# Performance work log

Hardware: AMD Instinct MI355X
Metric: run time of the kernel (lower is better)

## Reference

```python
import jax, jax.numpy as jnp
import numpy as np

NUM_CLASSES = 2
KS = 5  # kernel_size
EPS = 1e-8  # torch cosine_similarity eps


def setup_inputs() -> dict:
    key = jax.random.key(0)
    k1, k2, k3 = jax.random.split(key, 3)
    b, c, h, w = 8, 256, 128, 128
    er_input = jax.random.normal(k1, (b, c, h, w), dtype=jnp.float32)
    seg_label = jax.random.randint(k2, (b, h, w), 0, 2, dtype=jnp.int32)
    gt_boundary_seg = jax.random.randint(k3, (b, h, w), 0, 2, dtype=jnp.int32)
    return {"er_input": er_input, "seg_label": seg_label, "gt_boundary_seg": gt_boundary_seg}


def _context_loss(er_input, seg_label, gt_boundary_seg):
    # seg_label / gt_boundary_seg already at er_input spatial size (nearest interp is identity)
    b, c, h, w = er_input.shape
    r = KS // 2
    seg0 = jnp.where(seg_label == 255, 0, seg_label)
    gtb0 = jnp.where(gt_boundary_seg == 255, 0, gt_boundary_seg)
    gt_b = gtb0 * seg0                                  # [b,h,w] boundary pixels on fg classes
    interior = jnp.zeros((h, w), bool).at[r:h - r, r:w - r].set(True)
    valid = (gt_b > 0) & interior                       # pixels whose 5x5 window is in-bounds
    include = (gt_b > 0).any(axis=(1, 2))               # images contributing to scale_num
    cnt = valid.sum(axis=(1, 2)).astype(er_input.dtype)  # [b]

    norm = jnp.maximum(jnp.sqrt((er_input * er_input).sum(axis=1)), EPS)  # [b,h,w]
    validf = valid.astype(er_input.dtype)
    total = jnp.zeros((b,), dtype=er_input.dtype)
    n_shift = 0
    for dy in range(-r, r + 1):
        for dx in range(-r, r + 1):
            if dy == 0 and dx == 0:
                continue
            n_shift += 1
            # value at p+ (dy,dx) brought to p; valid pixels are interior so no wrap issue
            feat_s = jnp.roll(er_input, (-dy, -dx), axis=(2, 3))
            norm_s = jnp.roll(norm, (-dy, -dx), axis=(1, 2))
            seg_s = jnp.roll(seg_label, (-dy, -dx), axis=(1, 2))
            dot = (er_input * feat_s).sum(axis=1)       # [b,h,w]
            cos = dot / (norm * norm_s)
            # one_hot(seg,256)[:num_classes] dot product == labels equal AND label < num_classes
            labsim = ((seg_label == seg_s) & (seg_label < NUM_CLASSES)).astype(er_input.dtype)
            sq = (cos - labsim) ** 2
            # mse_loss over selected boundary pixels of image i
            total = total + (sq * validf).sum(axis=(1, 2)) / jnp.maximum(cnt, 1.0)
    loss_i = total / float(n_shift)                     # per-image context_loss_pi / 24
    scale_num = jnp.maximum(include.sum(), 1)
    return (loss_i * include.astype(loss_i.dtype)).sum() / scale_num.astype(loss_i.dtype)


def reference(er_input, seg_label, gt_boundary_seg):
    return _context_loss(er_input, seg_label, gt_boundary_seg)
```

## Files before the change

### kernel.cpp

```cpp
#include <hip/hip_runtime.h>
#include <math.h>

#define BATCH 8
#define CH    256
#define H     128
#define W     128
#define PLANE (H * W)
#define NPIX  (BATCH * PLANE)
#define NSHIFT 12
#define NMAPS  13
#define NCHUNK 4
#define CPC    (CH / NCHUNK)
#define NZ4    (NMAPS * NPIX / 4)

static __device__ __constant__ int S_DY[NSHIFT] = {0,0,1,1,1,1,1,2,2,2,2,2};
static __device__ __constant__ int S_DX[NSHIFT] = {1,2,-2,-1,0,1,2,-2,-1,0,1,2};

#define NCORRB (BATCH * 32 * NCHUNK)
#define NSTATB (BATCH * 64)

__device__ __forceinline__ void fma4(float& acc, const float4& a, const float4& b) {
    acc = fmaf(a.x, b.x, acc);
    acc = fmaf(a.y, b.y, acc);
    acc = fmaf(a.z, b.z, acc);
    acc = fmaf(a.w, b.w, acc);
}

__global__ __launch_bounds__(256) void k_prep(float4* __restrict__ comb4,
                                              int* __restrict__ cnt,
                                              int* __restrict__ inc,
                                              float* __restrict__ out) {
    int i = blockIdx.x * 256 + threadIdx.x;
    if (i < NZ4) comb4[i] = make_float4(0.f, 0.f, 0.f, 0.f);
    if (blockIdx.x == 0) {
        int t = threadIdx.x;
        if (t < 8) { cnt[t] = 0; inc[t] = 0; }
        if (t == 0) out[0] = 0.0f;
    }
}

__global__ __launch_bounds__(256, 4) void k_corr(const float* __restrict__ er,
                                                 const int* __restrict__ seg,
                                                 const int* __restrict__ gtb,
                                                 float* __restrict__ comb,
                                                 int* __restrict__ cnt,
                                                 int* __restrict__ inc) {
    __shared__ float4 lds[6][132];
    int t = threadIdx.x;

    if (blockIdx.x >= NCORRB) {
        int blk2 = blockIdx.x - NCORRB;
        int b = blk2 >> 6;
        int i = (blk2 & 63) * 256 + t;
        int my_cnt = 0, my_any = 0;
        {
            int s = seg[b * PLANE + i];
            int g = gtb[b * PLANE + i];
            int s0 = (s == 255) ? 0 : s;
            int g0 = (g == 255) ? 0 : g;
            if (s0 > 0 && g0 > 0) {
                my_any = 1;
                int y = i >> 7, x = i & 127;
                if (y >= 2 && y < H - 2 && x >= 2 && x < W - 2) my_cnt = 1;
            }
        }
        for (int o = 32; o > 0; o >>= 1) {
            my_cnt += __shfl_down(my_cnt, o, 64);
            my_any |= __shfl_down(my_any, o, 64);
        }
        __shared__ int sc[4], sa[4];
        int lane = t & 63, wid = t >> 6;
        if (lane == 0) { sc[wid] = my_cnt; sa[wid] = my_any; }
        __syncthreads();
        if (t == 0) {
            int c = sc[0] + sc[1] + sc[2] + sc[3];
            int a = sa[0] | sa[1] | sa[2] | sa[3];
            if (c) atomicAdd(&cnt[b], c);
            if (a) atomicOr(&inc[b], 1);
        }
        return;
    }

    int blk = blockIdx.x;
    int chunk = blk & 3;
    int tile  = (blk >> 2) & 31;
    int b     = blk >> 7;
    int y0 = tile * 4;
    int c0 = chunk * CPC;
    int r = t >> 7;
    int x = t & 127;

    if (t < 24) {
        int row = t >> 2, col = t & 3;
        int xs = (col < 2) ? col : (col + 128);
        lds[row][xs] = make_float4(0.f, 0.f, 0.f, 0.f);
    }

    float accA[13], accB[13];
#pragma unroll
    for (int i = 0; i < 13; i++) { accA[i] = 0.0f; accB[i] = 0.0f; }

    const float* base = er + (size_t)b * CH * PLANE;

    float pf[3][4];
    auto load_quad = [&](int c) {
#pragma unroll
        for (int k = 0; k < 3; ++k) {
            int s = t + k * 256;
            int row = s >> 7;
            int xs = s & 127;
            int y = y0 + row;
            if (y < H) {
                const float* p0 = base + (size_t)c * PLANE + y * W + xs;
                pf[k][0] = p0[0];
                pf[k][1] = p0[PLANE];
                pf[k][2] = p0[2 * PLANE];
                pf[k][3] = p0[3 * PLANE];
            } else {
                pf[k][0] = 0.f; pf[k][1] = 0.f; pf[k][2] = 0.f; pf[k][3] = 0.f;
            }
        }
    };

    load_quad(c0);
    const int iters = CPC / 4;
    for (int it = 0; it < iters; ++it) {
        __syncthreads();
#pragma unroll
        for (int k = 0; k < 3; ++k) {
            int s = t + k * 256;
            int row = s >> 7;
            int xs = s & 127;
            lds[row][xs + 2] = make_float4(pf[k][0], pf[k][1], pf[k][2], pf[k][3]);
        }
        __syncthreads();
        if (it + 1 < iters) load_quad(c0 + 4 * (it + 1));

        const float4* lp = &lds[2 * r][x + 2];
        float4 cA = lp[0];
        float4 cB = lp[132];
        {
            float4 v1 = lp[1], v2 = lp[2];
            fma4(accA[0], cA, cA);
            fma4(accA[1], cA, v1);
            fma4(accA[2], cA, v2);
        }
        {
            float4 m2 = lp[130], m1 = lp[131], p1 = lp[133], p2 = lp[134];
            fma4(accA[3], cA, m2);
            fma4(accA[4], cA, m1);
            fma4(accA[5], cA, cB);
            fma4(accA[6], cA, p1);
            fma4(accA[7], cA, p2);
            fma4(accB[0], cB, cB);
            fma4(accB[1], cB, p1);
            fma4(accB[2], cB, p2);
        }
        {
            float4 m2 = lp[262], m1 = lp[263], v0 = lp[264], p1 = lp[265], p2 = lp[266];
            fma4(accA[8],  cA, m2);
            fma4(accA[9],  cA, m1);
            fma4(accA[10], cA, v0);
            fma4(accA[11], cA, p1);
            fma4(accA[12], cA, p2);
            fma4(accB[3], cB, m2);
            fma4(accB[4], cB, m1);
            fma4(accB[5], cB, v0);
            fma4(accB[6], cB, p1);
            fma4(accB[7], cB, p2);
        }
        {
            float4 m2 = lp[394], m1 = lp[395], v0 = lp[396], p1 = lp[397], p2 = lp[398];
            fma4(accB[8],  cB, m2);
            fma4(accB[9],  cB, m1);
            fma4(accB[10], cB, v0);
            fma4(accB[11], cB, p1);
            fma4(accB[12], cB, p2);
        }
    }

    int pixA = b * PLANE + (y0 + 2 * r) * W + x;
    int pixB = pixA + W;
#pragma unroll
    for (int m = 0; m < NSHIFT; ++m) {
        atomicAdd(&comb[m * NPIX + pixA], accA[m + 1]);
        atomicAdd(&comb[m * NPIX + pixB], accB[m + 1]);
    }
    atomicAdd(&comb[NSHIFT * NPIX + pixA], accA[0]);
    atomicAdd(&comb[NSHIFT * NPIX + pixB], accB[0]);
}

__global__ __launch_bounds__(256) void k_loss(const float* __restrict__ comb,
                                              const int* __restrict__ seg,
                                              const int* __restrict__ gtb,
                                              const int* __restrict__ cnt,
                                              const int* __restrict__ inc,
                                              float* __restrict__ out) {
    const float* dots   = comb;
    const float* normsq = comb + NSHIFT * NPIX;
    int idx = blockIdx.x * 256 + threadIdx.x;
    int b = idx >> 14;
    int rem = idx & (PLANE - 1);
    int y = rem >> 7;
    int x = rem & 127;

    int sn = 0;
#pragma unroll
    for (int b2 = 0; b2 < BATCH; b2++) sn += (inc[b2] != 0);
    if (sn < 1) sn = 1;
    int cb = cnt[b]; if (cb < 1) cb = 1;
    float factor = inc[b] ? 1.0f / (24.0f * (float)cb * (float)sn) : 0.0f;

    float val = 0.0f;
    if (y >= 2 && y < H - 2 && x >= 2 && x < W - 2) {
        int sp = seg[idx];
        int gp = gtb[idx];
        int s0 = (sp == 255) ? 0 : sp;
        int g0 = (gp == 255) ? 0 : gp;
        if (s0 > 0 && g0 > 0) {
            float np = fmaxf(sqrtf(normsq[idx]), 1e-8f);
            float sum = 0.0f;
#pragma unroll
            for (int i = 0; i < NSHIFT; ++i) {
                int off = S_DY[i] * W + S_DX[i];
                {
                    float d  = dots[i * NPIX + idx];
                    float nn = fmaxf(sqrtf(normsq[idx + off]), 1e-8f);
                    float cosv = d / (np * nn);
                    int sq = seg[idx + off];
                    float lab = (sp == sq && sp < 2) ? 1.0f : 0.0f;
                    float tt = cosv - lab;
                    sum = fmaf(tt, tt, sum);
                }
                {
                    float d  = dots[i * NPIX + idx - off];
                    float nn = fmaxf(sqrtf(normsq[idx - off]), 1e-8f);
                    float cosv = d / (np * nn);
                    int sq = seg[idx - off];
                    float lab = (sp == sq && sp < 2) ? 1.0f : 0.0f;
                    float tt = cosv - lab;
                    sum = fmaf(tt, tt, sum);
                }
            }
            val = sum * factor;
        }
    }

    for (int o = 32; o > 0; o >>= 1)
        val += __shfl_down(val, o, 64);
    __shared__ float wsum[4];
    int lane = threadIdx.x & 63;
    int wid  = threadIdx.x >> 6;
    if (lane == 0) wsum[wid] = val;
    __syncthreads();
    if (threadIdx.x == 0) {
        float s = wsum[0] + wsum[1] + wsum[2] + wsum[3];
        atomicAdd(out, s);
    }
}

extern "C" void kernel_launch(void* const* d_in, const int* in_sizes, int n_in,
                              void* d_out, int out_size, void* d_ws, size_t ws_size,
                              hipStream_t stream) {
    const float* er  = (const float*)d_in[0];
    const int*   seg = (const int*)d_in[1];
    const int*   gtb = (const int*)d_in[2];
    float* out = (float*)d_out;

    float* ws   = (float*)d_ws;
    float* comb = ws;
    int*   cnt  = (int*)(comb + NMAPS * NPIX);
    int*   inc  = cnt + 8;

    hipLaunchKernelGGL(k_prep, dim3((NZ4 + 255) / 256), dim3(256), 0, stream,
                       (float4*)comb, cnt, inc, out);
    hipLaunchKernelGGL(k_corr, dim3(NCORRB + NSTATB), dim3(256), 0, stream,
                       er, seg, gtb, comb, cnt, inc);
    hipLaunchKernelGGL(k_loss, dim3(NPIX / 256), dim3(256), 0, stream,
                       comb, seg, gtb, cnt, inc, out);
}
```

Before: 221.3 us.

## Compute four output rows per thread with 8-row tiles and 8 channel chunks

Each thread now accumulates 4 output rows instead of 2, over 8-row tiles with a 2-row halo, so each block stages 10 LDS rows rather than 6. This cuts halo reload overhead and LDS reads per FMA. The channel dimension is split into 8 chunks instead of 4 to keep the block count the same. The trade-off is twice as many atomicAdd partial sums into the combined maps, more registers (52 accumulators, launch bounds lowered to 3), and more LDS per block.

New measurement: 235.1 us. 1.06x slower.

```diff
diff --git a/kernel.cpp b/kernel.cpp
--- a/kernel.cpp
+++ b/kernel.cpp
@@ -9,14 +9,16 @@
 #define NPIX  (BATCH * PLANE)
 #define NSHIFT 12
 #define NMAPS  13
-#define NCHUNK 4
+#define NCHUNK 8
 #define CPC    (CH / NCHUNK)
+#define TROWS  8
+#define NTILE  (H / TROWS)
 #define NZ4    (NMAPS * NPIX / 4)
 
 static __device__ __constant__ int S_DY[NSHIFT] = {0,0,1,1,1,1,1,2,2,2,2,2};
 static __device__ __constant__ int S_DX[NSHIFT] = {1,2,-2,-1,0,1,2,-2,-1,0,1,2};
 
-#define NCORRB (BATCH * 32 * NCHUNK)
+#define NCORRB (BATCH * NTILE * NCHUNK)
 #define NSTATB (BATCH * 64)
 
 __device__ __forceinline__ void fma4(float& acc, const float4& a, const float4& b) {
@@ -39,13 +41,13 @@
     }
 }
 
-__global__ __launch_bounds__(256, 4) void k_corr(const float* __restrict__ er,
+__global__ __launch_bounds__(256, 3) void k_corr(const float* __restrict__ er,
                                                  const int* __restrict__ seg,
                                                  const int* __restrict__ gtb,
                                                  float* __restrict__ comb,
                                                  int* __restrict__ cnt,
                                                  int* __restrict__ inc) {
-    __shared__ float4 lds[6][132];
+    __shared__ float4 lds[10][132];
     int t = threadIdx.x;
 
     if (blockIdx.x >= NCORRB) {
@@ -82,30 +84,32 @@
     }
 
     int blk = blockIdx.x;
-    int chunk = blk & 3;
-    int tile  = (blk >> 2) & 31;
+    int chunk = blk & 7;
+    int tile  = (blk >> 3) & 15;
     int b     = blk >> 7;
-    int y0 = tile * 4;
+    int y0 = tile * TROWS;
     int c0 = chunk * CPC;
     int r = t >> 7;
     int x = t & 127;
 
-    if (t < 24) {
+    if (t < 40) {
         int row = t >> 2, col = t & 3;
         int xs = (col < 2) ? col : (col + 128);
         lds[row][xs] = make_float4(0.f, 0.f, 0.f, 0.f);
     }
 
-    float accA[13], accB[13];
-#pragma unroll
-    for (int i = 0; i < 13; i++) { accA[i] = 0.0f; accB[i] = 0.0f; }
+    float acc[4][13];
+#pragma unroll
+    for (int o = 0; o < 4; ++o)
+#pragma unroll
+        for (int m = 0; m < 13; ++m) acc[o][m] = 0.0f;
 
     const float* base = er + (size_t)b * CH * PLANE;
 
-    float pf[3][4];
+    float pf[5][4];
     auto load_quad = [&](int c) {
 #pragma unroll
-        for (int k = 0; k < 3; ++k) {
+        for (int k = 0; k < 5; ++k) {
             int s = t + k * 256;
             int row = s >> 7;
             int xs = s & 127;
@@ -126,68 +130,58 @@
     const int iters = CPC / 4;
     for (int it = 0; it < iters; ++it) {
         __syncthreads();
-#pragma unroll
-        for (int k = 0; k < 3; ++k) {
+        float4* lf = (float4*)lds;
+#pragma unroll
+        for (int k = 0; k < 5; ++k) {
             int s = t + k * 256;
             int row = s >> 7;
             int xs = s & 127;
-            lds[row][xs + 2] = make_float4(pf[k][0], pf[k][1], pf[k][2], pf[k][3]);
+            lf[row * 132 + xs + 2] = make_float4(pf[k][0], pf[k][1], pf[k][2], pf[k][3]);
         }
         __syncthreads();
         if (it + 1 < iters) load_quad(c0 + 4 * (it + 1));
 
-        const float4* lp = &lds[2 * r][x + 2];
-        float4 cA = lp[0];
-        float4 cB = lp[132];
-        {
-            float4 v1 = lp[1], v2 = lp[2];
-            fma4(accA[0], cA, cA);
-            fma4(accA[1], cA, v1);
-            fma4(accA[2], cA, v2);
-        }
-        {
-            float4 m2 = lp[130], m1 = lp[131], p1 = lp[133], p2 = lp[134];
-            fma4(accA[3], cA, m2);
-            fma4(accA[4], cA, m1);
-            fma4(accA[5], cA, cB);
-            fma4(accA[6], cA, p1);
-            fma4(accA[7], cA, p2);
-            fma4(accB[0], cB, cB);
-            fma4(accB[1], cB, p1);
-            fma4(accB[2], cB, p2);
-        }
-        {
-            float4 m2 = lp[262], m1 = lp[263], v0 = lp[264], p1 = lp[265], p2 = lp[266];
-            fma4(accA[8],  cA, m2);
-            fma4(accA[9],  cA, m1);
-            fma4(accA[10], cA, v0);
-            fma4(accA[11], cA, p1);
-            fma4(accA[12], cA, p2);
-            fma4(accB[3], cB, m2);
-            fma4(accB[4], cB, m1);
-            fma4(accB[5], cB, v0);
-            fma4(accB[6], cB, p1);
-            fma4(accB[7], cB, p2);
-        }
-        {
-            float4 m2 = lp[394], m1 = lp[395], v0 = lp[396], p1 = lp[397], p2 = lp[398];
-            fma4(accB[8],  cB, m2);
-            fma4(accB[9],  cB, m1);
-            fma4(accB[10], cB, v0);
-            fma4(accB[11], cB, p1);
-            fma4(accB[12], cB, p2);
-        }
-    }
-
-    int pixA = b * PLANE + (y0 + 2 * r) * W + x;
-    int pixB = pixA + W;
-#pragma unroll
-    for (int m = 0; m < NSHIFT; ++m) {
-        atomicAdd(&comb[m * NPIX + pixA], accA[m + 1]);
-        atomicAdd(&comb[m * NPIX + pixB], accB[m + 1]);
-    }
-    atomicAdd(&comb[NSHIFT * NPIX + pixA], accA[0]);
-    atomicAdd(&comb[NSHIFT * NPIX + pixB], accB[0]);
+        const float4* colp = &lds[4 * r][x + 2];
+        float4 cen[4];
+#pragma unroll
+        for (int j = 0; j < 6; ++j) {
+            const float4* row = colp + j * 132;
+            float4 c0v = row[0], p1 = row[1], p2 = row[2];
+            float4 m1 = make_float4(0.f,0.f,0.f,0.f), m2 = m1;
+            if (j >= 1) { m1 = row[-1]; m2 = row[-2]; }
+            if (j < 4) {
+                cen[j] = c0v;
+                fma4(acc[j][12], c0v, c0v);
+                fma4(acc[j][0],  c0v, p1);
+                fma4(acc[j][1],  c0v, p2);
+            }
+            if (j >= 1 && j <= 4) {
+                float4 a = cen[j - 1];
+                fma4(acc[j-1][2], a, m2);
+                fma4(acc[j-1][3], a, m1);
+                fma4(acc[j-1][4], a, c0v);
+                fma4(acc[j-1][5], a, p1);
+                fma4(acc[j-1][6], a, p2);
+            }
+            if (j >= 2) {
+                float4 a = cen[j - 2];
+                fma4(acc[j-2][7],  a, m2);
+                fma4(acc[j-2][8],  a, m1);
+                fma4(acc[j-2][9],  a, c0v);
+                fma4(acc[j-2][10], a, p1);
+                fma4(acc[j-2][11], a, p2);
+            }
+        }
+    }
+
+#pragma unroll
+    for (int o = 0; o < 4; ++o) {
+        int pix = b * PLANE + (y0 + 4 * r + o) * W + x;
+#pragma unroll
+        for (int m = 0; m < NSHIFT; ++m)
+            atomicAdd(&comb[m * NPIX + pix], acc[o][m]);
+        atomicAdd(&comb[NSHIFT * NPIX + pix], acc[o][12]);
+    }
 }
 
 __global__ __launch_bounds__(256) void k_loss(const float* __restrict__ comb,
```

## Process four pixels per thread in loss kernel and split channels into eight chunks

Applied to the files above, without the earlier changes.

The loss kernel now handles four adjacent pixels per thread. It loads vectorised rows of seg, normsq and dot maps and reuses neighbour norms and labels across the four pixels, which cuts scattered scalar loads and repeated sqrt work. The correlation kernel splits channels into eight chunks instead of four, giving more blocks for occupancy at the cost of twice as many atomic adds into the maps. The accumulator indices are renumbered so the norm map is stored last, and the loss kernel computes all pixels unconditionally and masks invalid ones afterwards.

Result: slower. 233.0 us (+5.3%).

```diff
diff --git a/kernel.cpp b/kernel.cpp
--- a/kernel.cpp
+++ b/kernel.cpp
@@ -9,12 +9,10 @@
 #define NPIX  (BATCH * PLANE)
 #define NSHIFT 12
 #define NMAPS  13
-#define NCHUNK 4
+#define NCHUNK 8
 #define CPC    (CH / NCHUNK)
 #define NZ4    (NMAPS * NPIX / 4)
 
-static __device__ __constant__ int S_DY[NSHIFT] = {0,0,1,1,1,1,1,2,2,2,2,2};
-static __device__ __constant__ int S_DX[NSHIFT] = {1,2,-2,-1,0,1,2,-2,-1,0,1,2};
 
 #define NCORRB (BATCH * 32 * NCHUNK)
 #define NSTATB (BATCH * 64)
@@ -82,9 +80,9 @@
     }
 
     int blk = blockIdx.x;
-    int chunk = blk & 3;
-    int tile  = (blk >> 2) & 31;
-    int b     = blk >> 7;
+    int chunk = blk & 7;
+    int tile  = (blk >> 3) & 31;
+    int b     = blk >> 8;
     int y0 = tile * 4;
     int c0 = chunk * CPC;
     int r = t >> 7;
@@ -141,53 +139,68 @@
         float4 cB = lp[132];
         {
             float4 v1 = lp[1], v2 = lp[2];
-            fma4(accA[0], cA, cA);
-            fma4(accA[1], cA, v1);
-            fma4(accA[2], cA, v2);
+            fma4(accA[12], cA, cA);
+            fma4(accA[0],  cA, v1);
+            fma4(accA[1],  cA, v2);
         }
         {
             float4 m2 = lp[130], m1 = lp[131], p1 = lp[133], p2 = lp[134];
-            fma4(accA[3], cA, m2);
-            fma4(accA[4], cA, m1);
-            fma4(accA[5], cA, cB);
-            fma4(accA[6], cA, p1);
-            fma4(accA[7], cA, p2);
-            fma4(accB[0], cB, cB);
-            fma4(accB[1], cB, p1);
-            fma4(accB[2], cB, p2);
+            fma4(accA[2], cA, m2);
+            fma4(accA[3], cA, m1);
+            fma4(accA[4], cA, cB);
+            fma4(accA[5], cA, p1);
+            fma4(accA[6], cA, p2);
+            fma4(accB[12], cB, cB);
+            fma4(accB[0],  cB, p1);
+            fma4(accB[1],  cB, p2);
         }
         {
             float4 m2 = lp[262], m1 = lp[263], v0 = lp[264], p1 = lp[265], p2 = lp[266];
-            fma4(accA[8],  cA, m2);
-            fma4(accA[9],  cA, m1);
-            fma4(accA[10], cA, v0);
-            fma4(accA[11], cA, p1);
-            fma4(accA[12], cA, p2);
-            fma4(accB[3], cB, m2);
-            fma4(accB[4], cB, m1);
-            fma4(accB[5], cB, v0);
-            fma4(accB[6], cB, p1);
-            fma4(accB[7], cB, p2);
+            fma4(accA[7],  cA, m2);
+            fma4(accA[8],  cA, m1);
+            fma4(accA[9],  cA, v0);
+            fma4(accA[10], cA, p1);
+            fma4(accA[11], cA, p2);
+            fma4(accB[2], cB, m2);
+            fma4(accB[3], cB, m1);
+            fma4(accB[4], cB, v0);
+            fma4(accB[5], cB, p1);
+            fma4(accB[6], cB, p2);
         }
         {
             float4 m2 = lp[394], m1 = lp[395], v0 = lp[396], p1 = lp[397], p2 = lp[398];
-            fma4(accB[8],  cB, m2);
-            fma4(accB[9],  cB, m1);
-            fma4(accB[10], cB, v0);
-            fma4(accB[11], cB, p1);
-            fma4(accB[12], cB, p2);
+            fma4(accB[7],  cB, m2);
+            fma4(accB[8],  cB, m1);
+            fma4(accB[9],  cB, v0);
+            fma4(accB[10], cB, p1);
+            fma4(accB[11], cB, p2);
         }
     }
 
     int pixA = b * PLANE + (y0 + 2 * r) * W + x;
     int pixB = pixA + W;
 #pragma unroll
-    for (int m = 0; m < NSHIFT; ++m) {
-        atomicAdd(&comb[m * NPIX + pixA], accA[m + 1]);
-        atomicAdd(&comb[m * NPIX + pixB], accB[m + 1]);
-    }
-    atomicAdd(&comb[NSHIFT * NPIX + pixA], accA[0]);
-    atomicAdd(&comb[NSHIFT * NPIX + pixB], accB[0]);
+    for (int m = 0; m < NMAPS; ++m) {
+        atomicAdd(&comb[m * NPIX + pixA], accA[m]);
+        atomicAdd(&comb[m * NPIX + pixB], accB[m]);
+    }
+}
+
+__device__ __forceinline__ void ldrow_f(const float* p, int x0, float a[12]) {
+    float4 u = *((const float4*)(x0 == 0   ? p : p - 4));
+    float4 v = *((const float4*)p);
+    float4 w = *((const float4*)(x0 == 124 ? p : p + 4));
+    a[0]=u.x; a[1]=u.y; a[2]=u.z; a[3]=u.w;
+    a[4]=v.x; a[5]=v.y; a[6]=v.z; a[7]=v.w;
+    a[8]=w.x; a[9]=w.y; a[10]=w.z; a[11]=w.w;
+}
+__device__ __forceinline__ void ldrow_i(const int* p, int x0, int a[12]) {
+    int4 u = *((const int4*)(x0 == 0   ? p : p - 4));
+    int4 v = *((const int4*)p);
+    int4 w = *((const int4*)(x0 == 124 ? p : p + 4));
+    a[0]=u.x; a[1]=u.y; a[2]=u.z; a[3]=u.w;
+    a[4]=v.x; a[5]=v.y; a[6]=v.z; a[7]=v.w;
+    a[8]=w.x; a[9]=w.y; a[10]=w.z; a[11]=w.w;
 }
 
 __global__ __launch_bounds__(256) void k_loss(const float* __restrict__ comb,
@@ -198,11 +211,11 @@
                                               float* __restrict__ out) {
     const float* dots   = comb;
     const float* normsq = comb + NSHIFT * NPIX;
-    int idx = blockIdx.x * 256 + threadIdx.x;
-    int b = idx >> 14;
-    int rem = idx & (PLANE - 1);
+    int idx0 = (blockIdx.x * 256 + threadIdx.x) * 4;
+    int b = idx0 >> 14;
+    int rem = idx0 & (PLANE - 1);
     int y = rem >> 7;
-    int x = rem & 127;
+    int x0 = rem & 127;
 
     int sn = 0;
 #pragma unroll
@@ -212,38 +225,92 @@
     float factor = inc[b] ? 1.0f / (24.0f * (float)cb * (float)sn) : 0.0f;
 
     float val = 0.0f;
-    if (y >= 2 && y < H - 2 && x >= 2 && x < W - 2) {
-        int sp = seg[idx];
-        int gp = gtb[idx];
-        int s0 = (sp == 255) ? 0 : sp;
-        int g0 = (gp == 255) ? 0 : gp;
-        if (s0 > 0 && g0 > 0) {
-            float np = fmaxf(sqrtf(normsq[idx]), 1e-8f);
-            float sum = 0.0f;
-#pragma unroll
-            for (int i = 0; i < NSHIFT; ++i) {
-                int off = S_DY[i] * W + S_DX[i];
-                {
-                    float d  = dots[i * NPIX + idx];
-                    float nn = fmaxf(sqrtf(normsq[idx + off]), 1e-8f);
-                    float cosv = d / (np * nn);
-                    int sq = seg[idx + off];
-                    float lab = (sp == sq && sp < 2) ? 1.0f : 0.0f;
+    if (y >= 2 && y <= H - 3) {
+        int4 sc4 = *((const int4*)(seg + idx0));
+        int4 gc4 = *((const int4*)(gtb + idx0));
+        int sp[4] = {sc4.x, sc4.y, sc4.z, sc4.w};
+        int gp[4] = {gc4.x, gc4.y, gc4.z, gc4.w};
+        float4 nc4 = *((const float4*)(normsq + idx0));
+        float ncv[4] = {nc4.x, nc4.y, nc4.z, nc4.w};
+        float np[4], sum[4];
+        bool vld[4];
+#pragma unroll
+        for (int j = 0; j < 4; ++j) {
+            int s0 = (sp[j] == 255) ? 0 : sp[j];
+            int g0 = (gp[j] == 255) ? 0 : gp[j];
+            int xj = x0 + j;
+            vld[j] = (s0 > 0 && g0 > 0 && xj >= 2 && xj <= W - 3);
+            np[j] = fmaxf(sqrtf(ncv[j]), 1e-8f);
+            sum[j] = 0.0f;
+        }
+
+        {
+            int sr0[12];
+            float nr0[12], nn0[12];
+            ldrow_i(seg + idx0, x0, sr0);
+            ldrow_f(normsq + idx0, x0, nr0);
+#pragma unroll
+            for (int k = 0; k < 12; ++k) nn0[k] = fmaxf(sqrtf(nr0[k]), 1e-8f);
+#pragma unroll
+            for (int dx = 1; dx <= 2; ++dx) {
+                int i = dx - 1;
+                float dr[12];
+                ldrow_f(dots + (size_t)i * NPIX + idx0, x0, dr);
+#pragma unroll
+                for (int j = 0; j < 4; ++j) {
+                    float lab = (sp[j] == sr0[j + dx + 4] && sp[j] < 2) ? 1.f : 0.f;
+                    float cosv = dr[j + 4] / (np[j] * nn0[j + dx + 4]);
                     float tt = cosv - lab;
-                    sum = fmaf(tt, tt, sum);
+                    sum[j] = fmaf(tt, tt, sum[j]);
+                    float lab2 = (sp[j] == sr0[j - dx + 4] && sp[j] < 2) ? 1.f : 0.f;
+                    float cos2 = dr[j - dx + 4] / (np[j] * nn0[j - dx + 4]);
+                    float t2 = cos2 - lab2;
+                    sum[j] = fmaf(t2, t2, sum[j]);
                 }
-                {
-                    float d  = dots[i * NPIX + idx - off];
-                    float nn = fmaxf(sqrtf(normsq[idx - off]), 1e-8f);
-                    float cosv = d / (np * nn);
-                    int sq = seg[idx - off];
-                    float lab = (sp == sq && sp < 2) ? 1.0f : 0.0f;
+            }
+        }
+#pragma unroll
+        for (int d = 1; d <= 2; ++d) {
+            int mb = (d == 1) ? 2 : 7;
+            int srp[12], srm[12];
+            float nnp[12], nnm[12];
+            ldrow_i(seg + idx0 + d * W, x0, srp);
+            ldrow_i(seg + idx0 - d * W, x0, srm);
+            {
+                float tp[12], tm[12];
+                ldrow_f(normsq + idx0 + d * W, x0, tp);
+                ldrow_f(normsq + idx0 - d * W, x0, tm);
+#pragma unroll
+                for (int k = 0; k < 12; ++k) {
+                    nnp[k] = fmaxf(sqrtf(tp[k]), 1e-8f);
+                    nnm[k] = fmaxf(sqrtf(tm[k]), 1e-8f);
+                }
+            }
+#pragma unroll
+            for (int dx = -2; dx <= 2; ++dx) {
+                int i = mb + dx + 2;
+                float4 dc = *((const float4*)(dots + (size_t)i * NPIX + idx0));
+                float dcv[4] = {dc.x, dc.y, dc.z, dc.w};
+                float drm[12];
+                ldrow_f(dots + (size_t)i * NPIX + idx0 - d * W, x0, drm);
+#pragma unroll
+                for (int j = 0; j < 4; ++j) {
+                    float lab = (sp[j] == srp[j + dx + 4] && sp[j] < 2) ? 1.f : 0.f;
+                    float cosv = dcv[j] / (np[j] * nnp[j + dx + 4]);
                     float tt = cosv - lab;
-                    sum = fmaf(tt, tt, sum);
+                    sum[j] = fmaf(tt, tt, sum[j]);
+                    float lab2 = (sp[j] == srm[j - dx + 4] && sp[j] < 2) ? 1.f : 0.f;
+                    float cos2 = drm[j - dx + 4] / (np[j] * nnm[j - dx + 4]);
+                    float t2 = cos2 - lab2;
+                    sum[j] = fmaf(t2, t2, sum[j]);
                 }
             }
-            val = sum * factor;
-        }
+        }
+
+        float s = 0.0f;
+#pragma unroll
+        for (int j = 0; j < 4; ++j) s += vld[j] ? sum[j] : 0.0f;
+        val = s * factor;
     }
 
     for (int o = 32; o > 0; o >>= 1)
@@ -276,6 +343,6 @@
                        (float4*)comb, cnt, inc, out);
     hipLaunchKernelGGL(k_corr, dim3(NCORRB + NSTATB), dim3(256), 0, stream,
                        er, seg, gtb, comb, cnt, inc);
-    hipLaunchKernelGGL(k_loss, dim3(NPIX / 256), dim3(256), 0, stream,
+    hipLaunchKernelGGL(k_loss, dim3(NPIX / 4 / 256), dim3(256), 0, stream,
                        comb, seg, gtb, cnt, inc, out);
 }
```
